# Kernel tuning notes

Hardware: AMD Instinct MI355X
Metric: run time of the kernel (lower is better)

## Reference

```python
import jax, jax.numpy as jnp
import numpy as np

B, S, HID, NH, DH, L, FF = 1, 4096, 768, 12, 64, 12, 3072
WIN = 256       # one-sided sliding window (attention_window = 512 total)
NG = 16         # number of global-attention tokens
VOCAB = 50265
NEG = -1e9


def layer_norm(x, g, b, eps=1e-5):
    mu = jnp.mean(x, -1, keepdims=True)
    var = jnp.mean((x - mu) ** 2, -1, keepdims=True)
    return (x - mu) * jax.lax.rsqrt(var + eps) * g + b


def forward(input_ids, attention_mask, global_attention_mask, tok_emb, pos_emb,
            emb_ln_w, emb_ln_b, Wqkv, bqkv, Wo, bo, ln1_w, ln1_b,
            W1, b1, W2, b2, ln2_w, ln2_b, cls_W, cls_b):
    c = WIN
    nc = S // c
    amask = attention_mask.astype(jnp.float32)          # [B,S]
    gmask = global_attention_mask.astype(jnp.float32)   # [B,S]

    # --- static-shape helpers for the sparse pattern ---
    # key chunk k covers padded positions [k*c, k*c + 3c)
    idx = (jnp.arange(nc) * c)[:, None] + jnp.arange(3 * c)[None, :]      # [nc,3c]
    diff = jnp.arange(3 * c)[None, :] - c - jnp.arange(c)[:, None]        # [c,3c]
    band = jnp.abs(diff) <= c
    mp = jnp.pad(amask, ((0, 0), (c, c)))[:, idx]                         # [B,nc,3c]
    gp = jnp.pad(gmask, ((0, 0), (c, c)))[:, idx]
    key_ok = (mp > 0) & (gp == 0)           # local keys: valid and not global (globals handled separately)
    loc_valid = band[None, None] & key_ok[:, :, None, :]                  # [B,nc,c,3c]

    # indices of the NG global tokens (earliest first)
    _, gidx = jax.lax.top_k(gmask * (2.0 * S) - jnp.arange(S, dtype=jnp.float32), NG)
    gvalid = jnp.take_along_axis(gmask, gidx, axis=1)                     # [B,NG]

    def attn(x, Wqkv_l, bqkv_l, Wo_l, bo_l):
        qkv = x @ Wqkv_l + bqkv_l
        q, k, v = jnp.split(qkv, 3, axis=-1)
        hd = lambda t: t.reshape(B, S, NH, DH).transpose(0, 2, 1, 3)      # [B,nh,S,dh]
        q = hd(q) * (DH ** -0.5); k = hd(k); v = hd(v)

        # sliding-window (banded) attention via overlapping key chunks
        kp = jnp.pad(k, ((0, 0), (0, 0), (c, c), (0, 0)))
        vp = jnp.pad(v, ((0, 0), (0, 0), (c, c), (0, 0)))
        Kc, Vc = kp[:, :, idx], vp[:, :, idx]                             # [B,nh,nc,3c,dh]
        Qc = q.reshape(B, NH, nc, c, DH)
        s_loc = jnp.einsum('bhkpd,bhkqd->bhkpq', Qc, Kc)                  # [B,nh,nc,c,3c]
        s_loc = jnp.where(loc_valid[:, None], s_loc, NEG)

        # every token also attends to the global tokens
        gi = jnp.broadcast_to(gidx[:, None, :, None], (B, NH, NG, DH))
        Kg = jnp.take_along_axis(k, gi, axis=2)                           # [B,nh,NG,dh]
        Vg = jnp.take_along_axis(v, gi, axis=2)
        Qg = jnp.take_along_axis(q, gi, axis=2)
        s_glb = jnp.einsum('bhkpd,bhgd->bhkpg', Qc, Kg)                   # [B,nh,nc,c,NG]
        s_glb = jnp.where(gvalid[:, None, None, None, :] > 0, s_glb, NEG)

        p = jax.nn.softmax(jnp.concatenate([s_loc, s_glb], -1), axis=-1)
        o = (jnp.einsum('bhkpq,bhkqd->bhkpd', p[..., :3 * c], Vc)
             + jnp.einsum('bhkpg,bhgd->bhkpd', p[..., 3 * c:], Vg))
        o = o.reshape(B, NH, S, DH).transpose(0, 2, 1, 3)                 # [B,S,nh,dh]

        # global tokens attend to the full sequence
        s_full = jnp.einsum('bhgd,bhsd->bhgs', Qg, k)
        s_full = jnp.where(amask[:, None, None, :] > 0, s_full, NEG)
        og = jnp.einsum('bhgs,bhsd->bhgd', jax.nn.softmax(s_full, -1), v)
        og = og.transpose(0, 2, 1, 3)                                     # [B,NG,nh,dh]
        bi = jnp.arange(B)[:, None]
        o = o.at[bi, gidx].set(jnp.where(gvalid[..., None, None] > 0, og, o[bi, gidx]))
        return o.reshape(B, S, HID) @ Wo_l + bo_l

    h = layer_norm(tok_emb[input_ids] + pos_emb[None], emb_ln_w, emb_ln_b)

    def step(h, p):
        Wq, bq, Wo_l, bo_l, g1, bl1, w1, bb1, w2, bb2, g2, bl2 = p
        h = layer_norm(h + attn(h, Wq, bq, Wo_l, bo_l), g1, bl1)          # post-LN, RoBERTa-style
        f = jax.nn.gelu(h @ w1 + bb1, approximate=False) @ w2 + bb2
        h = layer_norm(h + f, g2, bl2)
        return h, None

    h, _ = jax.lax.scan(step, h, (Wqkv, bqkv, Wo, bo, ln1_w, ln1_b,
                                  W1, b1, W2, b2, ln2_w, ln2_b))
    m = amask[..., None]
    pooled = (h * m).sum(1) / m.sum(1)           # masked mean-pool; dropout is eval no-op
    return pooled @ cls_W + cls_b                # [B,2] logits


def setup_inputs():
    key = jax.random.key(0)
    ks = jax.random.split(key, 8)
    nrm = lambda k, shp: jax.random.normal(k, shp, jnp.float32) * 0.02
    return dict(
        input_ids=jax.random.randint(ks[0], (B, S), 0, VOCAB),
        attention_mask=jnp.ones((B, S), jnp.int32),
        global_attention_mask=jnp.concatenate(
            [jnp.ones((B, NG), jnp.int32), jnp.zeros((B, S - NG), jnp.int32)], axis=1),
        tok_emb=nrm(ks[1], (VOCAB, HID)),
        pos_emb=nrm(ks[2], (S, HID)),
        emb_ln_w=jnp.ones((HID,)), emb_ln_b=jnp.zeros((HID,)),
        Wqkv=nrm(ks[3], (L, HID, 3 * HID)), bqkv=jnp.zeros((L, 3 * HID)),
        Wo=nrm(ks[4], (L, HID, HID)), bo=jnp.zeros((L, HID)),
        ln1_w=jnp.ones((L, HID)), ln1_b=jnp.zeros((L, HID)),
        W1=nrm(ks[5], (L, HID, FF)), b1=jnp.zeros((L, FF)),
        W2=nrm(ks[6], (L, FF, HID)), b2=jnp.zeros((L, HID)),
        ln2_w=jnp.ones((L, HID)), ln2_b=jnp.zeros((L, HID)),
        cls_W=nrm(ks[7], (HID, 2)), cls_b=jnp.zeros((2,)),
    )


def reference(input_ids, attention_mask, global_attention_mask, tok_emb, pos_emb,
              emb_ln_w, emb_ln_b, Wqkv, bqkv, Wo, bo, ln1_w, ln1_b,
              W1, b1, W2, b2, ln2_w, ln2_b, cls_W, cls_b):
    return forward(input_ids, attention_mask, global_attention_mask, tok_emb, pos_emb,
                   emb_ln_w, emb_ln_b, Wqkv, bqkv, Wo, bo, ln1_w, ln1_b,
                   W1, b1, W2, b2, ln2_w, ln2_b, cls_W, cls_b)
```

## Files before the change

kernel.cpp:

```cpp
#include <hip/hip_runtime.h>
#include <cmath>

#define S 4096
#define HID 768
#define NH 12
#define DH 64
#define CHUNK 256
#define NC (S / CHUNK)
#define NG 16
#define FF 3072
#define NLAYER 12
#define QKV3 (3 * HID)
#define NEGV -1e9f

typedef _Float16 f16;
typedef __attribute__((ext_vector_type(2))) _Float16 f16x2;
typedef __attribute__((ext_vector_type(4))) _Float16 f16x4;
typedef __attribute__((ext_vector_type(8))) _Float16 f16x8;
typedef __attribute__((ext_vector_type(4))) float f32x4;

__device__ __forceinline__ void async16(f16* lds, const f16* g) {
  __builtin_amdgcn_global_load_lds((const __attribute__((address_space(1))) unsigned int*)g,
                                   (__attribute__((address_space(3))) unsigned int*)lds,
                                   16, 0, 0);
}

__device__ __forceinline__ int xcd_swz(int lin, int nwg) {
  return (lin & 7) * (nwg >> 3) + (lin >> 3);
}

__device__ __forceinline__ float block_reduce_sum(float v, float* red) {
  int t = threadIdx.x;
  red[t] = v; __syncthreads();
  for (int st = 128; st > 0; st >>= 1) {
    if (t < st) red[t] += red[t + st];
    __syncthreads();
  }
  float r = red[0]; __syncthreads();
  return r;
}

__global__ void gidx_kernel(const int* __restrict__ gmask, int* __restrict__ gidx,
                            float* __restrict__ gvalid) {
  if (threadIdx.x != 0 || blockIdx.x != 0) return;
  int cnt = 0;
  for (int s = 0; s < S && cnt < NG; s++)
    if (gmask[s] > 0) { gidx[cnt] = s; gvalid[cnt] = 1.f; cnt++; }
  for (int s = 0; s < S && cnt < NG; s++)
    if (gmask[s] == 0) { gidx[cnt] = s; gvalid[cnt] = 0.f; cnt++; }
}

__global__ __launch_bounds__(256) void embed_ln_kernel(
    const int* __restrict__ ids, const float* __restrict__ tok,
    const float* __restrict__ pos, const float* __restrict__ g,
    const float* __restrict__ b, float* __restrict__ h, f16* __restrict__ h16) {
  int s = blockIdx.x, t = threadIdx.x;
  __shared__ float xs[HID];
  __shared__ float red[256];
  const float* tr = tok + (size_t)ids[s] * HID;
  const float* pr = pos + (size_t)s * HID;
  float ls = 0.f;
  for (int i = t; i < HID; i += 256) { float v = tr[i] + pr[i]; xs[i] = v; ls += v; }
  float mu = block_reduce_sum(ls, red) * (1.f / HID);
  float lv = 0.f;
  for (int i = t; i < HID; i += 256) { float d = xs[i] - mu; lv += d * d; }
  float var = block_reduce_sum(lv, red) * (1.f / HID);
  float inv = rsqrtf(var + 1e-5f);
  for (int i = t; i < HID; i += 256) {
    float o = (xs[i] - mu) * inv * g[i] + b[i];
    h[(size_t)s * HID + i] = o;
    h16[(size_t)s * HID + i] = (f16)o;
  }
}

__global__ __launch_bounds__(256) void add_ln_kernel(
    float* __restrict__ h, const f16* __restrict__ x2,
    const float* __restrict__ g, const float* __restrict__ b, f16* __restrict__ h16) {
  int s = blockIdx.x, t = threadIdx.x;
  __shared__ float xs[HID];
  __shared__ float red[256];
  float ls = 0.f;
  for (int i = t; i < HID; i += 256) {
    float v = h[(size_t)s * HID + i] + (float)x2[(size_t)s * HID + i];
    xs[i] = v; ls += v;
  }
  float mu = block_reduce_sum(ls, red) * (1.f / HID);
  float lv = 0.f;
  for (int i = t; i < HID; i += 256) { float d = xs[i] - mu; lv += d * d; }
  float var = block_reduce_sum(lv, red) * (1.f / HID);
  float inv = rsqrtf(var + 1e-5f);
  for (int i = t; i < HID; i += 256) {
    float o = (xs[i] - mu) * inv * g[i] + b[i];
    h[(size_t)s * HID + i] = o;
    h16[(size_t)s * HID + i] = (f16)o;
  }
}

__global__ __launch_bounds__(256) void wt_kernel(const float* __restrict__ W,
                                                 f16* __restrict__ WT, int K, int N) {
  size_t lo = (size_t)blockIdx.z * K * N;
  const float* Wl = W + lo;
  f16* WTl = WT + lo;
  __shared__ float tile[32][33];
  int k0 = blockIdx.y * 32, n0 = blockIdx.x * 32;
  int t = threadIdx.x;
  int r = t >> 3, c = (t & 7) * 4;
  float4 v = *(const float4*)&Wl[(size_t)(k0 + r) * N + n0 + c];
  tile[r][c] = v.x; tile[r][c + 1] = v.y; tile[r][c + 2] = v.z; tile[r][c + 3] = v.w;
  __syncthreads();
  int n = t >> 3, kq = (t & 7) * 4;
  f16x4 o = {(f16)tile[kq][n], (f16)tile[kq + 1][n], (f16)tile[kq + 2][n], (f16)tile[kq + 3][n]};
  *(f16x4*)&WTl[(size_t)(n0 + n) * K + k0 + kq] = o;
}

#define GBK 64

template <int OMODE, bool GELU>
__global__ __launch_bounds__(256) void gemm_f16_kernel(
    const f16* __restrict__ A, const f16* __restrict__ BT,
    const float* __restrict__ bias, void* __restrict__ Cout, int M, int N, int K) {
  __shared__ f16 As[128 * GBK];
  __shared__ f16 Bs[128 * GBK];
  int t = threadIdx.x, lane = t & 63, wave = t >> 6;
  int wr = wave >> 1, wc = wave & 1;
  int gx = gridDim.x;
  int nl = xcd_swz(blockIdx.y * gx + blockIdx.x, gx * gridDim.y);
  int bx = nl % gx, by = nl / gx;

  f32x4 acc[4][4];
#pragma unroll
  for (int mi = 0; mi < 4; mi++)
#pragma unroll
    for (int ni = 0; ni < 4; ni++) acc[mi][ni] = (f32x4){0.f, 0.f, 0.f, 0.f};

  const f16* Ablk = A + (size_t)(by * 128) * K;
  const f16* Bblk = BT + (size_t)(bx * 128) * K;
  int rl = lane >> 3;
  int lc = (lane & 7) ^ rl;

  for (int k0 = 0; k0 < K; k0 += GBK) {
#pragma unroll
    for (int ii = 0; ii < 4; ii++) {
      int i = wave * 4 + ii;
      int r = i * 8 + rl;
      async16(&As[i * 512], Ablk + (size_t)r * K + k0 + lc * 8);
      async16(&Bs[i * 512], Bblk + (size_t)r * K + k0 + lc * 8);
    }
    __syncthreads();
#pragma unroll
    for (int kc = 0; kc < 2; kc++) {
      f16x8 af[4], bf[4];
#pragma unroll
      for (int mi = 0; mi < 4; mi++) {
        int row = wr * 64 + mi * 16 + (lane & 15);
        int pc = (kc * 4 + (lane >> 4)) ^ (row & 7);
        af[mi] = *(const f16x8*)&As[row * 64 + pc * 8];
      }
#pragma unroll
      for (int ni = 0; ni < 4; ni++) {
        int row = wc * 64 + ni * 16 + (lane & 15);
        int pc = (kc * 4 + (lane >> 4)) ^ (row & 7);
        bf[ni] = *(const f16x8*)&Bs[row * 64 + pc * 8];
      }
#pragma unroll
      for (int mi = 0; mi < 4; mi++)
#pragma unroll
        for (int ni = 0; ni < 4; ni++)
          acc[mi][ni] = __builtin_amdgcn_mfma_f32_16x16x32_f16(af[mi], bf[ni], acc[mi][ni], 0, 0, 0);
    }
    __syncthreads();
  }

  int row_base = by * 128 + wr * 64 + (lane >> 4) * 4;
  int col_base = bx * 128 + wc * 64 + (lane & 15);
#pragma unroll
  for (int mi = 0; mi < 4; mi++) {
#pragma unroll
    for (int ni = 0; ni < 4; ni++) {
      int col = col_base + ni * 16;
      float bs = bias[col];
#pragma unroll
      for (int j = 0; j < 4; j++) {
        int row = row_base + mi * 16 + j;
        float x = acc[mi][ni][j] + bs;
        if (GELU) x = 0.5f * x * (1.f + erff(x * 0.70710678118654752f));
        if (OMODE == 0) ((float*)Cout)[(size_t)row * N + col] = x;
        else ((f16*)Cout)[(size_t)row * N + col] = (f16)x;
      }
    }
  }
}

template <int OMODE, bool GELU>
__global__ __launch_bounds__(256) void gemm_f16_n64_kernel(
    const f16* __restrict__ A, const f16* __restrict__ BT,
    const float* __restrict__ bias, void* __restrict__ Cout, int M, int N, int K) {
  __shared__ f16 As[128 * GBK];
  __shared__ f16 Bs[64 * GBK];
  int t = threadIdx.x, lane = t & 63, wave = t >> 6;
  int wr = wave >> 1, wc = wave & 1;
  int gx = gridDim.x;
  int nl = xcd_swz(blockIdx.y * gx + blockIdx.x, gx * gridDim.y);
  int bx = nl % gx, by = nl / gx;

  f32x4 acc[4][2];
#pragma unroll
  for (int mi = 0; mi < 4; mi++)
#pragma unroll
    for (int ni = 0; ni < 2; ni++) acc[mi][ni] = (f32x4){0.f, 0.f, 0.f, 0.f};

  const f16* Ablk = A + (size_t)(by * 128) * K;
  const f16* Bblk = BT + (size_t)(bx * 64) * K;
  int rl = lane >> 3;
  int lc = (lane & 7) ^ rl;

  for (int k0 = 0; k0 < K; k0 += GBK) {
#pragma unroll
    for (int ii = 0; ii < 4; ii++) {
      int i = wave * 4 + ii;
      int r = i * 8 + rl;
      async16(&As[i * 512], Ablk + (size_t)r * K + k0 + lc * 8);
    }
#pragma unroll
    for (int ii = 0; ii < 2; ii++) {
      int i = wave * 2 + ii;
      int r = i * 8 + rl;
      async16(&Bs[i * 512], Bblk + (size_t)r * K + k0 + lc * 8);
    }
    __syncthreads();
#pragma unroll
    for (int kc = 0; kc < 2; kc++) {
      f16x8 af[4], bf[2];
#pragma unroll
      for (int mi = 0; mi < 4; mi++) {
        int row = wr * 64 + mi * 16 + (lane & 15);
        int pc = (kc * 4 + (lane >> 4)) ^ (row & 7);
        af[mi] = *(const f16x8*)&As[row * 64 + pc * 8];
      }
#pragma unroll
      for (int ni = 0; ni < 2; ni++) {
        int row = wc * 32 + ni * 16 + (lane & 15);
        int pc = (kc * 4 + (lane >> 4)) ^ (row & 7);
        bf[ni] = *(const f16x8*)&Bs[row * 64 + pc * 8];
      }
#pragma unroll
      for (int mi = 0; mi < 4; mi++)
#pragma unroll
        for (int ni = 0; ni < 2; ni++)
          acc[mi][ni] = __builtin_amdgcn_mfma_f32_16x16x32_f16(af[mi], bf[ni], acc[mi][ni], 0, 0, 0);
    }
    __syncthreads();
  }

  int row_base = by * 128 + wr * 64 + (lane >> 4) * 4;
  int col_base = bx * 64 + wc * 32 + (lane & 15);
#pragma unroll
  for (int mi = 0; mi < 4; mi++) {
#pragma unroll
    for (int ni = 0; ni < 2; ni++) {
      int col = col_base + ni * 16;
      float bs = bias[col];
#pragma unroll
      for (int j = 0; j < 4; j++) {
        int row = row_base + mi * 16 + j;
        float x = acc[mi][ni][j] + bs;
        if (GELU) x = 0.5f * x * (1.f + erff(x * 0.70710678118654752f));
        if (OMODE == 0) ((float*)Cout)[(size_t)row * N + col] = x;
        else ((f16*)Cout)[(size_t)row * N + col] = (f16)x;
      }
    }
  }
}

#define ROWP 72

__global__ __launch_bounds__(256) void local_attn_mfma_kernel(
    const f16* __restrict__ qkv, const int* __restrict__ amask,
    const int* __restrict__ gmask, const int* __restrict__ gidx,
    const float* __restrict__ gvalid, f16* __restrict__ outp) {
  int nl = xcd_swz(blockIdx.x, NH * 64);
  int h = nl >> 6;
  int qb = nl & 63;
  int q0 = qb * 64;
  int t = threadIdx.x, lane = t & 63, w = t >> 6;
  int g4 = lane >> 4, l15 = lane & 15;

  __shared__ f16 Qs[64 * ROWP];
  __shared__ f16 Kt[64 * ROWP];
  __shared__ f16 Vt[64 * ROWP];
  __shared__ f16 Pb[4 * 16 * ROWP];
  __shared__ unsigned kokLo, kokHi;
  __shared__ float gvs[NG];

  {
    int r = t >> 2, c2 = (t & 3) * 2;
    const f16* qr = qkv + (size_t)(q0 + r) * QKV3 + h * DH + c2 * 8;
    f16x8 v0 = *(const f16x8*)qr;
    f16x8 v1 = *(const f16x8*)(qr + 8);
#pragma unroll
    for (int e = 0; e < 8; e++) { v0[e] = v0[e] * (f16)0.125f; v1[e] = v1[e] * (f16)0.125f; }
    *(f16x8*)&Qs[r * ROWP + c2 * 8] = v0;
    *(f16x8*)&Qs[r * ROWP + c2 * 8 + 8] = v1;
    if (t < NG) gvs[t] = gvalid[t];
  }
  __syncthreads();

  int qrow = w * 16 + l15;
  f16x8 qf0 = *(const f16x8*)&Qs[qrow * ROWP + g4 * 8];
  f16x8 qf1 = *(const f16x8*)&Qs[qrow * ROWP + 32 + g4 * 8];

  float mb = -50000.f, lp = 0.f;
  f32x4 oacc[4];
#pragma unroll
  for (int sd = 0; sd < 4; sd++) oacc[sd] = (f32x4){0.f, 0.f, 0.f, 0.f};

  f16* Pw = &Pb[w * 16 * ROWP];

  for (int kt = 0; kt <= 9; kt++) {
    int jb = q0 - 256 + kt * 64;
    bool isG = (kt == 9);
    if (!isG && (jb + 64 <= 0 || jb >= S)) continue;
    __syncthreads();
    {
      int k = t >> 2, c2 = (t & 3) * 2;
      int j = isG ? (k < NG ? gidx[k] : -1) : (jb + k);
      bool jv = isG ? (k < NG && gvs[k] > 0.f) : (j >= 0 && j < S);
      f16x8 v0 = {}, v1 = {};
      if (jv) {
        const f16* kr = qkv + (size_t)j * QKV3 + HID + h * DH + c2 * 8;
        v0 = *(const f16x8*)kr; v1 = *(const f16x8*)(kr + 8);
      }
      *(f16x8*)&Kt[k * ROWP + c2 * 8] = v0;
      *(f16x8*)&Kt[k * ROWP + c2 * 8 + 8] = v1;
    }
    if (w == 0) {
      int k = lane;
      bool ok;
      if (isG) ok = (k < NG && gvs[k] > 0.f);
      else {
        int j = jb + k;
        ok = (j >= 0 && j < S) && (amask[j] != 0) && (gmask[j] == 0);
      }
      unsigned long long m = __ballot(ok);
      if (lane == 0) { kokLo = (unsigned)m; kokHi = (unsigned)(m >> 32); }
    }
    {
      int k2 = (t & 31) * 2, dq = (t >> 5) * 8;
      int j0 = isG ? (k2 < NG ? gidx[k2] : -1) : (jb + k2);
      int j1 = isG ? (k2 + 1 < NG ? gidx[k2 + 1] : -1) : (jb + k2 + 1);
      bool ok0 = isG ? (k2 < NG && gvs[k2] > 0.f) : (j0 >= 0 && j0 < S);
      bool ok1 = isG ? (k2 + 1 < NG && gvs[k2 + 1] > 0.f) : (j1 >= 0 && j1 < S);
      f16x8 va = {}, vb = {};
      if (ok0) va = *(const f16x8*)(qkv + (size_t)j0 * QKV3 + 2 * HID + h * DH + dq);
      if (ok1) vb = *(const f16x8*)(qkv + (size_t)j1 * QKV3 + 2 * HID + h * DH + dq);
#pragma unroll
      for (int e = 0; e < 8; e++) {
        f16x2 pr = {va[e], vb[e]};
        *(f16x2*)&Vt[(dq + e) * ROWP + k2] = pr;
      }
    }
    __syncthreads();

    unsigned long long kok = ((unsigned long long)kokHi << 32) | (unsigned long long)kokLo;

    f32x4 sv[4];
    __builtin_amdgcn_s_setprio(1);
#pragma unroll
    for (int s4 = 0; s4 < 4; s4++) {
      int krow = s4 * 16 + l15;
      f16x8 ka0 = *(const f16x8*)&Kt[krow * ROWP + g4 * 8];
      f16x8 ka1 = *(const f16x8*)&Kt[krow * ROWP + 32 + g4 * 8];
      f32x4 a = {0.f, 0.f, 0.f, 0.f};
      a = __builtin_amdgcn_mfma_f32_16x16x32_f16(ka0, qf0, a, 0, 0, 0);
      a = __builtin_amdgcn_mfma_f32_16x16x32_f16(ka1, qf1, a, 0, 0, 0);
      sv[s4] = a;
    }
    __builtin_amdgcn_s_setprio(0);
    int ql = w * 16 + l15;
#pragma unroll
    for (int s4 = 0; s4 < 4; s4++)
#pragma unroll
      for (int r = 0; r < 4; r++) {
        int kl = s4 * 16 + g4 * 4 + r;
        bool ok = (kok >> kl) & 1ull;
        if (kt == 0) ok = ok && (kl >= ql);
        else if (kt == 8) ok = ok && (kl <= ql);
        sv[s4][r] = ok ? sv[s4][r] : -1e30f;
      }
    float mt = -1e30f;
#pragma unroll
    for (int s4 = 0; s4 < 4; s4++)
#pragma unroll
      for (int r = 0; r < 4; r++) mt = fmaxf(mt, sv[s4][r]);
    mt = fmaxf(mt, __shfl_xor(mt, 16));
    mt = fmaxf(mt, __shfl_xor(mt, 32));
    float mn = fmaxf(mb, mt);
    float corr = __expf(mb - mn);
    mb = mn;
    lp *= corr;
#pragma unroll
    for (int sd = 0; sd < 4; sd++)
#pragma unroll
      for (int r = 0; r < 4; r++) oacc[sd][r] *= corr;
#pragma unroll
    for (int s4 = 0; s4 < 4; s4++) {
#pragma unroll
      for (int rp = 0; rp < 2; rp++) {
        float p0 = __expf(sv[s4][rp * 2] - mn);
        float p1 = __expf(sv[s4][rp * 2 + 1] - mn);
        f16 h0 = (f16)p0, h1 = (f16)p1;
        lp += (float)h0 + (float)h1;
        int kl = s4 * 16 + g4 * 4 + rp * 2;
        f16x2 pr = {h0, h1};
        *(f16x2*)&Pw[l15 * ROWP + kl] = pr;
      }
    }
    f16x8 pf0 = *(const f16x8*)&Pw[l15 * ROWP + g4 * 8];
    f16x8 pf1 = *(const f16x8*)&Pw[l15 * ROWP + 32 + g4 * 8];
    __builtin_amdgcn_s_setprio(1);
#pragma unroll
    for (int sd = 0; sd < 4; sd++) {
      int drow = sd * 16 + l15;
      f16x8 va0 = *(const f16x8*)&Vt[drow * ROWP + g4 * 8];
      f16x8 va1 = *(const f16x8*)&Vt[drow * ROWP + 32 + g4 * 8];
      oacc[sd] = __builtin_amdgcn_mfma_f32_16x16x32_f16(va0, pf0, oacc[sd], 0, 0, 0);
      oacc[sd] = __builtin_amdgcn_mfma_f32_16x16x32_f16(va1, pf1, oacc[sd], 0, 0, 0);
    }
    __builtin_amdgcn_s_setprio(0);
  }

  float lt = lp + __shfl_xor(lp, 16);
  lt = lt + __shfl_xor(lt, 32);
  float inv = (lt > 0.f) ? 1.f / lt : 0.f;
  int qg = q0 + w * 16 + l15;
  f16* orow = outp + (size_t)qg * HID + h * DH;
#pragma unroll
  for (int sd = 0; sd < 4; sd++)
#pragma unroll
    for (int r = 0; r < 4; r++)
      orow[sd * 16 + g4 * 4 + r] = (f16)(oacc[sd][r] * inv);
}

__global__ __launch_bounds__(256) void gscore_kernel(
    const f16* __restrict__ qkv, const int* __restrict__ amask,
    const int* __restrict__ gidx, float* __restrict__ Sg, float2* __restrict__ cstat) {
  int h = blockIdx.x >> 4, jc = blockIdx.x & 15;
  int t = threadIdx.x, lane = t & 63, w = t >> 6;
  __shared__ f16 Qs[NG][DH];
  __shared__ float wred[4][NG];
  __shared__ float cmaxs[NG];
  if (t < 128) {
    int g = t >> 3, c = (t & 7) * 8;
    const f16* qr = qkv + (size_t)gidx[g] * QKV3 + h * DH + c;
    *(f16x8*)&Qs[g][c] = *(const f16x8*)qr;
  }
  __syncthreads();
  int j = jc * 256 + t;
  const f16x8* kr = (const f16x8*)(qkv + (size_t)j * QKV3 + HID + h * DH);
  f16x8 kv[8];
#pragma unroll
  for (int c = 0; c < 8; c++) kv[c] = kr[c];
  bool ok = amask[j] != 0;
  float sg[NG];
#pragma unroll 4
  for (int g = 0; g < NG; g++) {
    float s = 0.f;
#pragma unroll
    for (int c = 0; c < 8; c++) {
      f16x8 qv = *(const f16x8*)&Qs[g][c * 8];
#pragma unroll
      for (int e = 0; e < 8; e++) s += (float)qv[e] * (float)kv[c][e];
    }
    sg[g] = ok ? s * 0.125f : NEGV;
    Sg[(size_t)(h * NG + g) * S + j] = sg[g];
  }
#pragma unroll
  for (int g = 0; g < NG; g++) {
    float m = sg[g];
#pragma unroll
    for (int st = 1; st < 64; st <<= 1) m = fmaxf(m, __shfl_xor(m, st));
    if (lane == 0) wred[w][g] = m;
  }
  __syncthreads();
  if (t < NG)
    cmaxs[t] = fmaxf(fmaxf(wred[0][t], wred[1][t]), fmaxf(wred[2][t], wred[3][t]));
  __syncthreads();
#pragma unroll
  for (int g = 0; g < NG; g++) {
    float p = __expf(sg[g] - cmaxs[g]);
#pragma unroll
    for (int st = 1; st < 64; st <<= 1) p += __shfl_xor(p, st);
    if (lane == 0) wred[w][g] = p;
  }
  __syncthreads();
  if (t < NG) {
    float s4 = wred[0][t] + wred[1][t] + wred[2][t] + wred[3][t];
    cstat[((size_t)(h * NG + t)) * 16 + jc] = make_float2(cmaxs[t], s4);
  }
}

__global__ __launch_bounds__(256) void gpv_kernel(
    const f16* __restrict__ qkv, const float* __restrict__ Sg,
    const float2* __restrict__ cstat, float* __restrict__ part) {
  int h = blockIdx.x >> 4, jc = blockIdx.x & 15;
  int jb = jc * 256;
  int t = threadIdx.x;
  __shared__ float Ps[NG][256];
  __shared__ f16 Vs[256][DH];
  __shared__ float ms[NG], dinv[NG];
  if (t < NG) {
    const float2* cs = &cstat[((size_t)(h * NG + t)) * 16];
    float m = -1e30f;
#pragma unroll
    for (int c = 0; c < 16; c++) m = fmaxf(m, cs[c].x);
    float den = 0.f;
#pragma unroll
    for (int c = 0; c < 16; c++) den += cs[c].y * __expf(cs[c].x - m);
    ms[t] = m;
    dinv[t] = den > 0.f ? 1.f / den : 0.f;
  }
  __syncthreads();
#pragma unroll
  for (int g = 0; g < NG; g++)
    Ps[g][t] = __expf(Sg[(size_t)(h * NG + g) * S + jb + t] - ms[g]) * dinv[g];
  {
    int r = t >> 3, c = (t & 7) * 8;
#pragma unroll
    for (int pp = 0; pp < 8; pp++) {
      int row = pp * 32 + r;
      const f16* vr = qkv + (size_t)(jb + row) * QKV3 + 2 * HID + h * DH + c;
      *(f16x8*)&Vs[row][c] = *(const f16x8*)vr;
    }
  }
  __syncthreads();
  int d = t & 63, g4 = t >> 6;
  float o0 = 0.f, o1 = 0.f, o2 = 0.f, o3 = 0.f;
#pragma unroll 8
  for (int j = 0; j < 256; j++) {
    float v = (float)Vs[j][d];
    o0 += Ps[g4][j] * v;
    o1 += Ps[g4 + 4][j] * v;
    o2 += Ps[g4 + 8][j] * v;
    o3 += Ps[g4 + 12][j] * v;
  }
  size_t base = ((size_t)h * NG) * 16 * 64;
  part[base + ((size_t)(g4) * 16 + jc) * 64 + d] = o0;
  part[base + ((size_t)(g4 + 4) * 16 + jc) * 64 + d] = o1;
  part[base + ((size_t)(g4 + 8) * 16 + jc) * 64 + d] = o2;
  part[base + ((size_t)(g4 + 12) * 16 + jc) * 64 + d] = o3;
}

__global__ __launch_bounds__(64) void gout_kernel(
    const float* __restrict__ part, const int* __restrict__ gidx,
    const float* __restrict__ gvalid, f16* __restrict__ attn16) {
  int h = blockIdx.x >> 4, g = blockIdx.x & 15;
  if (gvalid[g] <= 0.f) return;
  int d = threadIdx.x;
  const float* pr = part + (((size_t)(h * NG + g)) * 16) * 64 + d;
  float s = 0.f;
#pragma unroll
  for (int jc = 0; jc < 16; jc++) s += pr[jc * 64];
  attn16[(size_t)gidx[g] * HID + h * DH + d] = (f16)s;
}

__global__ __launch_bounds__(256) void pool_part_kernel(
    const float* __restrict__ h, const int* __restrict__ amask, float* __restrict__ part) {
  int b = blockIdx.x, t = threadIdx.x;
  float a0 = 0.f, a1 = 0.f, a2 = 0.f;
  for (int r = 0; r < 64; r++) {
    int s = b * 64 + r;
    float w = (float)amask[s];
    const float* hr = h + (size_t)s * HID;
    a0 += hr[t] * w;
    a1 += hr[t + 256] * w;
    a2 += hr[t + 512] * w;
  }
  part[(size_t)b * HID + t] = a0;
  part[(size_t)b * HID + t + 256] = a1;
  part[(size_t)b * HID + t + 512] = a2;
}

__global__ __launch_bounds__(256) void cls_head_kernel(
    const float* __restrict__ part, const int* __restrict__ amask,
    const float* __restrict__ clsW, const float* __restrict__ clsb,
    float* __restrict__ out) {
  __shared__ float pooled[HID];
  __shared__ float red[256];
  int t = threadIdx.x;
  for (int i = t; i < HID; i += 256) {
    float s = 0.f;
    for (int b2 = 0; b2 < 64; b2++) s += part[(size_t)b2 * HID + i];
    pooled[i] = s;
  }
  float c = 0.f;
  for (int s2 = t; s2 < S; s2 += 256) c += (float)amask[s2];
  float cnt = block_reduce_sum(c, red);
  float p0 = 0.f, p1 = 0.f;
  for (int i = t; i < HID; i += 256) {
    float pv = pooled[i] / cnt;
    p0 += pv * clsW[i * 2];
    p1 += pv * clsW[i * 2 + 1];
  }
  float s0 = block_reduce_sum(p0, red);
  float s1 = block_reduce_sum(p1, red);
  if (t == 0) { out[0] = s0 + clsb[0]; out[1] = s1 + clsb[1]; }
}

extern "C" void kernel_launch(void* const* d_in, const int* in_sizes, int n_in,
                              void* d_out, int out_size, void* d_ws, size_t ws_size,
                              hipStream_t stream) {
  const int* ids = (const int*)d_in[0];
  const int* amask = (const int*)d_in[1];
  const int* gmask = (const int*)d_in[2];
  const float* tok = (const float*)d_in[3];
  const float* pos = (const float*)d_in[4];
  const float* elnw = (const float*)d_in[5];
  const float* elnb = (const float*)d_in[6];
  const float* Wqkv = (const float*)d_in[7];
  const float* bqkv = (const float*)d_in[8];
  const float* Wo = (const float*)d_in[9];
  const float* bo = (const float*)d_in[10];
  const float* ln1w = (const float*)d_in[11];
  const float* ln1b = (const float*)d_in[12];
  const float* W1 = (const float*)d_in[13];
  const float* b1 = (const float*)d_in[14];
  const float* W2 = (const float*)d_in[15];
  const float* b2 = (const float*)d_in[16];
  const float* ln2w = (const float*)d_in[17];
  const float* ln2b = (const float*)d_in[18];
  const float* clsW = (const float*)d_in[19];
  const float* clsb = (const float*)d_in[20];

  char* w8 = (char*)d_ws;
  size_t o = 0;
  float* h = (float*)(w8 + o); o += (size_t)S * HID * 4;
  f16* h16 = (f16*)(w8 + o); o += (size_t)S * HID * 2;
  f16* qkv16 = (f16*)(w8 + o); o += (size_t)S * QKV3 * 2;
  f16* attn16 = (f16*)(w8 + o); o += (size_t)S * HID * 2;
  f16* ff16 = (f16*)(w8 + o); o += (size_t)S * FF * 2;
  f16* proj16 = (f16*)(w8 + o); o += (size_t)S * HID * 2;
  float* part = (float*)(w8 + o); o += (size_t)64 * HID * 4;
  int* gidx = (int*)(w8 + o); o += 64;
  float* gvalid = (float*)(w8 + o); o += 64;
  f16* WqkvT = (f16*)(w8 + o); o += (size_t)NLAYER * HID * QKV3 * 2;
  f16* WoT = (f16*)(w8 + o); o += (size_t)NLAYER * HID * HID * 2;
  f16* W1T = (f16*)(w8 + o); o += (size_t)NLAYER * HID * FF * 2;
  f16* W2T = (f16*)(w8 + o); o += (size_t)NLAYER * FF * HID * 2;
  float* Sg = (float*)(w8 + o); o += (size_t)NH * NG * S * 4;
  float2* cstat = (float2*)(w8 + o); o += (size_t)NH * NG * 16 * 8;
  float* gpart = (float*)(w8 + o); o += (size_t)NH * NG * 16 * 64 * 4;

  gidx_kernel<<<1, 64, 0, stream>>>(gmask, gidx, gvalid);
  embed_ln_kernel<<<S, 256, 0, stream>>>(ids, tok, pos, elnw, elnb, h, h16);
  wt_kernel<<<dim3(QKV3 / 32, HID / 32, NLAYER), 256, 0, stream>>>(Wqkv, WqkvT, HID, QKV3);
  wt_kernel<<<dim3(HID / 32, HID / 32, NLAYER), 256, 0, stream>>>(Wo, WoT, HID, HID);
  wt_kernel<<<dim3(FF / 32, HID / 32, NLAYER), 256, 0, stream>>>(W1, W1T, HID, FF);
  wt_kernel<<<dim3(HID / 32, FF / 32, NLAYER), 256, 0, stream>>>(W2, W2T, FF, HID);

  for (int l = 0; l < NLAYER; l++) {
    gemm_f16_kernel<1, false><<<dim3(QKV3 / 128, S / 128), 256, 0, stream>>>(
        h16, WqkvT + (size_t)l * HID * QKV3, bqkv + (size_t)l * QKV3, qkv16, S, QKV3, HID);
    local_attn_mfma_kernel<<<NH * 64, 256, 0, stream>>>(
        qkv16, amask, gmask, gidx, gvalid, attn16);
    gscore_kernel<<<NH * 16, 256, 0, stream>>>(qkv16, amask, gidx, Sg, cstat);
    gpv_kernel<<<NH * 16, 256, 0, stream>>>(qkv16, Sg, cstat, gpart);
    gout_kernel<<<NH * NG, 64, 0, stream>>>(gpart, gidx, gvalid, attn16);
    gemm_f16_n64_kernel<1, false><<<dim3(HID / 64, S / 128), 256, 0, stream>>>(
        attn16, WoT + (size_t)l * HID * HID, bo + (size_t)l * HID, proj16, S, HID, HID);
    add_ln_kernel<<<S, 256, 0, stream>>>(h, proj16, ln1w + (size_t)l * HID,
                                         ln1b + (size_t)l * HID, h16);
    gemm_f16_kernel<1, true><<<dim3(FF / 128, S / 128), 256, 0, stream>>>(
        h16, W1T + (size_t)l * HID * FF, b1 + (size_t)l * FF, ff16, S, FF, HID);
    gemm_f16_n64_kernel<1, false><<<dim3(HID / 64, S / 128), 256, 0, stream>>>(
        ff16, W2T + (size_t)l * FF * HID, b2 + (size_t)l * HID, proj16, S, HID, FF);
    add_ln_kernel<<<S, 256, 0, stream>>>(h, proj16, ln2w + (size_t)l * HID,
                                         ln2b + (size_t)l * HID, h16);
  }
  pool_part_kernel<<<64, 256, 0, stream>>>(h, amask, part);
  cls_head_kernel<<<1, 256, 0, stream>>>(part, amask, clsW, clsb, (float*)d_out);
}
```

Baseline: 2.586 ms.

## Fuse residual into GEMM epilogue, merge attention kernels, drop fp32 hidden state

The residual add moves into the output-projection and FFN-down GEMM epilogues, and the fp32 hidden-state buffer is removed, so LayerNorm reads one fp16 sum. Local attention and global score computation now share one launch with a block-index split. The global PV and output reduction merge into one kernel that loops over all chunks per (head, global token). This removes several launches and the fp32 traffic, but holding the residual stream in fp16 across 12 layers adds rounding error, and the merged global PV kernel has less parallelism.

```diff
diff --git a/kernel.cpp b/kernel.cpp
--- a/kernel.cpp
+++ b/kernel.cpp
@@ -53,7 +53,7 @@
 __global__ __launch_bounds__(256) void embed_ln_kernel(
     const int* __restrict__ ids, const float* __restrict__ tok,
     const float* __restrict__ pos, const float* __restrict__ g,
-    const float* __restrict__ b, float* __restrict__ h, f16* __restrict__ h16) {
+    const float* __restrict__ b, f16* __restrict__ h16) {
   int s = blockIdx.x, t = threadIdx.x;
   __shared__ float xs[HID];
   __shared__ float red[256];
@@ -66,34 +66,25 @@
   for (int i = t; i < HID; i += 256) { float d = xs[i] - mu; lv += d * d; }
   float var = block_reduce_sum(lv, red) * (1.f / HID);
   float inv = rsqrtf(var + 1e-5f);
-  for (int i = t; i < HID; i += 256) {
-    float o = (xs[i] - mu) * inv * g[i] + b[i];
-    h[(size_t)s * HID + i] = o;
-    h16[(size_t)s * HID + i] = (f16)o;
-  }
-}
-
-__global__ __launch_bounds__(256) void add_ln_kernel(
-    float* __restrict__ h, const f16* __restrict__ x2,
-    const float* __restrict__ g, const float* __restrict__ b, f16* __restrict__ h16) {
+  for (int i = t; i < HID; i += 256)
+    h16[(size_t)s * HID + i] = (f16)((xs[i] - mu) * inv * g[i] + b[i]);
+}
+
+__global__ __launch_bounds__(256) void ln_kernel(
+    const f16* __restrict__ sum16, const float* __restrict__ g,
+    const float* __restrict__ b, f16* __restrict__ h16) {
   int s = blockIdx.x, t = threadIdx.x;
-  __shared__ float xs[HID];
   __shared__ float red[256];
-  float ls = 0.f;
-  for (int i = t; i < HID; i += 256) {
-    float v = h[(size_t)s * HID + i] + (float)x2[(size_t)s * HID + i];
-    xs[i] = v; ls += v;
-  }
-  float mu = block_reduce_sum(ls, red) * (1.f / HID);
-  float lv = 0.f;
-  for (int i = t; i < HID; i += 256) { float d = xs[i] - mu; lv += d * d; }
-  float var = block_reduce_sum(lv, red) * (1.f / HID);
+  float x0 = (float)sum16[(size_t)s * HID + t];
+  float x1 = (float)sum16[(size_t)s * HID + t + 256];
+  float x2 = (float)sum16[(size_t)s * HID + t + 512];
+  float mu = block_reduce_sum(x0 + x1 + x2, red) * (1.f / HID);
+  float d0 = x0 - mu, d1 = x1 - mu, d2 = x2 - mu;
+  float var = block_reduce_sum(d0 * d0 + d1 * d1 + d2 * d2, red) * (1.f / HID);
   float inv = rsqrtf(var + 1e-5f);
-  for (int i = t; i < HID; i += 256) {
-    float o = (xs[i] - mu) * inv * g[i] + b[i];
-    h[(size_t)s * HID + i] = o;
-    h16[(size_t)s * HID + i] = (f16)o;
-  }
+  h16[(size_t)s * HID + t] = (f16)(d0 * inv * g[t] + b[t]);
+  h16[(size_t)s * HID + t + 256] = (f16)(d1 * inv * g[t + 256] + b[t + 256]);
+  h16[(size_t)s * HID + t + 512] = (f16)(d2 * inv * g[t + 512] + b[t + 512]);
 }
 
 __global__ __launch_bounds__(256) void wt_kernel(const float* __restrict__ W,
@@ -115,10 +106,10 @@
 
 #define GBK 64
 
-template <int OMODE, bool GELU>
+template <bool GELU>
 __global__ __launch_bounds__(256) void gemm_f16_kernel(
     const f16* __restrict__ A, const f16* __restrict__ BT,
-    const float* __restrict__ bias, void* __restrict__ Cout, int M, int N, int K) {
+    const float* __restrict__ bias, f16* __restrict__ Cout, int M, int N, int K) {
   __shared__ f16 As[128 * GBK];
   __shared__ f16 Bs[128 * GBK];
   int t = threadIdx.x, lane = t & 63, wave = t >> 6;
@@ -184,17 +175,17 @@
         int row = row_base + mi * 16 + j;
         float x = acc[mi][ni][j] + bs;
         if (GELU) x = 0.5f * x * (1.f + erff(x * 0.70710678118654752f));
-        if (OMODE == 0) ((float*)Cout)[(size_t)row * N + col] = x;
-        else ((f16*)Cout)[(size_t)row * N + col] = (f16)x;
-      }
-    }
-  }
-}
-
-template <int OMODE, bool GELU>
+        Cout[(size_t)row * N + col] = (f16)x;
+      }
+    }
+  }
+}
+
+template <bool RESID>
 __global__ __launch_bounds__(256) void gemm_f16_n64_kernel(
     const f16* __restrict__ A, const f16* __restrict__ BT,
-    const float* __restrict__ bias, void* __restrict__ Cout, int M, int N, int K) {
+    const float* __restrict__ bias, const f16* __restrict__ resid,
+    f16* __restrict__ Cout, int M, int N, int K) {
   __shared__ f16 As[128 * GBK];
   __shared__ f16 Bs[64 * GBK];
   int t = threadIdx.x, lane = t & 63, wave = t >> 6;
@@ -264,316 +255,305 @@
       for (int j = 0; j < 4; j++) {
         int row = row_base + mi * 16 + j;
         float x = acc[mi][ni][j] + bs;
-        if (GELU) x = 0.5f * x * (1.f + erff(x * 0.70710678118654752f));
-        if (OMODE == 0) ((float*)Cout)[(size_t)row * N + col] = x;
-        else ((f16*)Cout)[(size_t)row * N + col] = (f16)x;
+        if (RESID) x += (float)resid[(size_t)row * N + col];
+        Cout[(size_t)row * N + col] = (f16)x;
       }
     }
   }
 }
 
 #define ROWP 72
-
-__global__ __launch_bounds__(256) void local_attn_mfma_kernel(
+#define SMEM_HALVES (4 * 4608 + 64)
+
+__global__ __launch_bounds__(256) void attn_fused_kernel(
     const f16* __restrict__ qkv, const int* __restrict__ amask,
     const int* __restrict__ gmask, const int* __restrict__ gidx,
-    const float* __restrict__ gvalid, f16* __restrict__ outp) {
-  int nl = xcd_swz(blockIdx.x, NH * 64);
-  int h = nl >> 6;
-  int qb = nl & 63;
-  int q0 = qb * 64;
+    const float* __restrict__ gvalid, f16* __restrict__ outp,
+    float* __restrict__ Sg, float2* __restrict__ cstat) {
+  __shared__ __align__(16) f16 smem[SMEM_HALVES];
+  int bid = blockIdx.x;
   int t = threadIdx.x, lane = t & 63, w = t >> 6;
-  int g4 = lane >> 4, l15 = lane & 15;
-
-  __shared__ f16 Qs[64 * ROWP];
-  __shared__ f16 Kt[64 * ROWP];
-  __shared__ f16 Vt[64 * ROWP];
-  __shared__ f16 Pb[4 * 16 * ROWP];
-  __shared__ unsigned kokLo, kokHi;
-  __shared__ float gvs[NG];
-
-  {
-    int r = t >> 2, c2 = (t & 3) * 2;
-    const f16* qr = qkv + (size_t)(q0 + r) * QKV3 + h * DH + c2 * 8;
-    f16x8 v0 = *(const f16x8*)qr;
-    f16x8 v1 = *(const f16x8*)(qr + 8);
-#pragma unroll
-    for (int e = 0; e < 8; e++) { v0[e] = v0[e] * (f16)0.125f; v1[e] = v1[e] * (f16)0.125f; }
-    *(f16x8*)&Qs[r * ROWP + c2 * 8] = v0;
-    *(f16x8*)&Qs[r * ROWP + c2 * 8 + 8] = v1;
-    if (t < NG) gvs[t] = gvalid[t];
-  }
-  __syncthreads();
-
-  int qrow = w * 16 + l15;
-  f16x8 qf0 = *(const f16x8*)&Qs[qrow * ROWP + g4 * 8];
-  f16x8 qf1 = *(const f16x8*)&Qs[qrow * ROWP + 32 + g4 * 8];
-
-  float mb = -50000.f, lp = 0.f;
-  f32x4 oacc[4];
-#pragma unroll
-  for (int sd = 0; sd < 4; sd++) oacc[sd] = (f32x4){0.f, 0.f, 0.f, 0.f};
-
-  f16* Pw = &Pb[w * 16 * ROWP];
-
-  for (int kt = 0; kt <= 9; kt++) {
-    int jb = q0 - 256 + kt * 64;
-    bool isG = (kt == 9);
-    if (!isG && (jb + 64 <= 0 || jb >= S)) continue;
-    __syncthreads();
+
+  if (bid < NH * 64) {
+    int nl = xcd_swz(bid, NH * 64);
+    int h = nl >> 6, qb = nl & 63;
+    int q0 = qb * 64;
+    int g4 = lane >> 4, l15 = lane & 15;
+
+    f16* Qs = smem;
+    f16* Kt = smem + 4608;
+    f16* Vt = smem + 2 * 4608;
+    f16* Pb = smem + 3 * 4608;
+    float* gvs = (float*)(smem + 4 * 4608);
+    unsigned* kokp = (unsigned*)(gvs + NG);
+
     {
-      int k = t >> 2, c2 = (t & 3) * 2;
-      int j = isG ? (k < NG ? gidx[k] : -1) : (jb + k);
-      bool jv = isG ? (k < NG && gvs[k] > 0.f) : (j >= 0 && j < S);
-      f16x8 v0 = {}, v1 = {};
-      if (jv) {
-        const f16* kr = qkv + (size_t)j * QKV3 + HID + h * DH + c2 * 8;
-        v0 = *(const f16x8*)kr; v1 = *(const f16x8*)(kr + 8);
-      }
-      *(f16x8*)&Kt[k * ROWP + c2 * 8] = v0;
-      *(f16x8*)&Kt[k * ROWP + c2 * 8 + 8] = v1;
-    }
-    if (w == 0) {
-      int k = lane;
-      bool ok;
-      if (isG) ok = (k < NG && gvs[k] > 0.f);
-      else {
-        int j = jb + k;
-        ok = (j >= 0 && j < S) && (amask[j] != 0) && (gmask[j] == 0);
-      }
-      unsigned long long m = __ballot(ok);
-      if (lane == 0) { kokLo = (unsigned)m; kokHi = (unsigned)(m >> 32); }
-    }
-    {
-      int k2 = (t & 31) * 2, dq = (t >> 5) * 8;
-      int j0 = isG ? (k2 < NG ? gidx[k2] : -1) : (jb + k2);
-      int j1 = isG ? (k2 + 1 < NG ? gidx[k2 + 1] : -1) : (jb + k2 + 1);
-      bool ok0 = isG ? (k2 < NG && gvs[k2] > 0.f) : (j0 >= 0 && j0 < S);
-      bool ok1 = isG ? (k2 + 1 < NG && gvs[k2 + 1] > 0.f) : (j1 >= 0 && j1 < S);
-      f16x8 va = {}, vb = {};
-      if (ok0) va = *(const f16x8*)(qkv + (size_t)j0 * QKV3 + 2 * HID + h * DH + dq);
-      if (ok1) vb = *(const f16x8*)(qkv + (size_t)j1 * QKV3 + 2 * HID + h * DH + dq);
-#pragma unroll
-      for (int e = 0; e < 8; e++) {
-        f16x2 pr = {va[e], vb[e]};
-        *(f16x2*)&Vt[(dq + e) * ROWP + k2] = pr;
-      }
-    }
-    __syncthreads();
-
-    unsigned long long kok = ((unsigned long long)kokHi << 32) | (unsigned long long)kokLo;
-
-    f32x4 sv[4];
-    __builtin_amdgcn_s_setprio(1);
-#pragma unroll
-    for (int s4 = 0; s4 < 4; s4++) {
-      int krow = s4 * 16 + l15;
-      f16x8 ka0 = *(const f16x8*)&Kt[krow * ROWP + g4 * 8];
-      f16x8 ka1 = *(const f16x8*)&Kt[krow * ROWP + 32 + g4 * 8];
-      f32x4 a = {0.f, 0.f, 0.f, 0.f};
-      a = __builtin_amdgcn_mfma_f32_16x16x32_f16(ka0, qf0, a, 0, 0, 0);
-      a = __builtin_amdgcn_mfma_f32_16x16x32_f16(ka1, qf1, a, 0, 0, 0);
-      sv[s4] = a;
-    }
-    __builtin_amdgcn_s_setprio(0);
-    int ql = w * 16 + l15;
-#pragma unroll
-    for (int s4 = 0; s4 < 4; s4++)
-#pragma unroll
-      for (int r = 0; r < 4; r++) {
-        int kl = s4 * 16 + g4 * 4 + r;
-        bool ok = (kok >> kl) & 1ull;
-        if (kt == 0) ok = ok && (kl >= ql);
-        else if (kt == 8) ok = ok && (kl <= ql);
-        sv[s4][r] = ok ? sv[s4][r] : -1e30f;
-      }
-    float mt = -1e30f;
-#pragma unroll
-    for (int s4 = 0; s4 < 4; s4++)
-#pragma unroll
-      for (int r = 0; r < 4; r++) mt = fmaxf(mt, sv[s4][r]);
-    mt = fmaxf(mt, __shfl_xor(mt, 16));
-    mt = fmaxf(mt, __shfl_xor(mt, 32));
-    float mn = fmaxf(mb, mt);
-    float corr = __expf(mb - mn);
-    mb = mn;
-    lp *= corr;
+      int r = t >> 2, c2 = (t & 3) * 2;
+      const f16* qr = qkv + (size_t)(q0 + r) * QKV3 + h * DH + c2 * 8;
+      f16x8 v0 = *(const f16x8*)qr;
+      f16x8 v1 = *(const f16x8*)(qr + 8);
+#pragma unroll
+      for (int e = 0; e < 8; e++) { v0[e] = v0[e] * (f16)0.125f; v1[e] = v1[e] * (f16)0.125f; }
+      *(f16x8*)&Qs[r * ROWP + c2 * 8] = v0;
+      *(f16x8*)&Qs[r * ROWP + c2 * 8 + 8] = v1;
+      if (t < NG) gvs[t] = gvalid[t];
+    }
+    __syncthreads();
+
+    int qrow = w * 16 + l15;
+    f16x8 qf0 = *(const f16x8*)&Qs[qrow * ROWP + g4 * 8];
+    f16x8 qf1 = *(const f16x8*)&Qs[qrow * ROWP + 32 + g4 * 8];
+
+    float mb = -50000.f, lp = 0.f;
+    f32x4 oacc[4];
+#pragma unroll
+    for (int sd = 0; sd < 4; sd++) oacc[sd] = (f32x4){0.f, 0.f, 0.f, 0.f};
+
+    f16* Pw = &Pb[w * 16 * ROWP];
+
+    for (int kt = 0; kt <= 9; kt++) {
+      int jb = q0 - 256 + kt * 64;
+      bool isG = (kt == 9);
+      if (!isG && (jb + 64 <= 0 || jb >= S)) continue;
+      __syncthreads();
+      {
+        int k = t >> 2, c2 = (t & 3) * 2;
+        int j = isG ? (k < NG ? gidx[k] : -1) : (jb + k);
+        bool jv = isG ? (k < NG && gvs[k] > 0.f) : (j >= 0 && j < S);
+        f16x8 v0 = {}, v1 = {};
+        if (jv) {
+          const f16* kr = qkv + (size_t)j * QKV3 + HID + h * DH + c2 * 8;
+          v0 = *(const f16x8*)kr; v1 = *(const f16x8*)(kr + 8);
+        }
+        *(f16x8*)&Kt[k * ROWP + c2 * 8] = v0;
+        *(f16x8*)&Kt[k * ROWP + c2 * 8 + 8] = v1;
+      }
+      if (w == 0) {
+        int k = lane;
+        bool ok;
+        if (isG) ok = (k < NG && gvs[k] > 0.f);
+        else {
+          int j = jb + k;
+          ok = (j >= 0 && j < S) && (amask[j] != 0) && (gmask[j] == 0);
+        }
+        unsigned long long m = __ballot(ok);
+        if (lane == 0) { kokp[0] = (unsigned)m; kokp[1] = (unsigned)(m >> 32); }
+      }
+      {
+        int k2 = (t & 31) * 2, dq = (t >> 5) * 8;
+        int j0 = isG ? (k2 < NG ? gidx[k2] : -1) : (jb + k2);
+        int j1 = isG ? (k2 + 1 < NG ? gidx[k2 + 1] : -1) : (jb + k2 + 1);
+        bool ok0 = isG ? (k2 < NG && gvs[k2] > 0.f) : (j0 >= 0 && j0 < S);
+        bool ok1 = isG ? (k2 + 1 < NG && gvs[k2 + 1] > 0.f) : (j1 >= 0 && j1 < S);
+        f16x8 va = {}, vb = {};
+        if (ok0) va = *(const f16x8*)(qkv + (size_t)j0 * QKV3 + 2 * HID + h * DH + dq);
+        if (ok1) vb = *(const f16x8*)(qkv + (size_t)j1 * QKV3 + 2 * HID + h * DH + dq);
+#pragma unroll
+        for (int e = 0; e < 8; e++) {
+          f16x2 pr = {va[e], vb[e]};
+          *(f16x2*)&Vt[(dq + e) * ROWP + k2] = pr;
+        }
+      }
+      __syncthreads();
+
+      unsigned long long kok = ((unsigned long long)kokp[1] << 32) | (unsigned long long)kokp[0];
+
+      f32x4 sv[4];
+      __builtin_amdgcn_s_setprio(1);
+#pragma unroll
+      for (int s4 = 0; s4 < 4; s4++) {
+        int krow = s4 * 16 + l15;
+        f16x8 ka0 = *(const f16x8*)&Kt[krow * ROWP + g4 * 8];
+        f16x8 ka1 = *(const f16x8*)&Kt[krow * ROWP + 32 + g4 * 8];
+        f32x4 a = {0.f, 0.f, 0.f, 0.f};
+        a = __builtin_amdgcn_mfma_f32_16x16x32_f16(ka0, qf0, a, 0, 0, 0);
+        a = __builtin_amdgcn_mfma_f32_16x16x32_f16(ka1, qf1, a, 0, 0, 0);
+        sv[s4] = a;
+      }
+      __builtin_amdgcn_s_setprio(0);
+      int ql = w * 16 + l15;
+#pragma unroll
+      for (int s4 = 0; s4 < 4; s4++)
+#pragma unroll
+        for (int r = 0; r < 4; r++) {
+          int kl = s4 * 16 + g4 * 4 + r;
+          bool ok = (kok >> kl) & 1ull;
+          if (kt == 0) ok = ok && (kl >= ql);
+          else if (kt == 8) ok = ok && (kl <= ql);
+          sv[s4][r] = ok ? sv[s4][r] : -1e30f;
+        }
+      float mt = -1e30f;
+#pragma unroll
+      for (int s4 = 0; s4 < 4; s4++)
+#pragma unroll
+        for (int r = 0; r < 4; r++) mt = fmaxf(mt, sv[s4][r]);
+      mt = fmaxf(mt, __shfl_xor(mt, 16));
+      mt = fmaxf(mt, __shfl_xor(mt, 32));
+      float mn = fmaxf(mb, mt);
+      float corr = __expf(mb - mn);
+      mb = mn;
+      lp *= corr;
+#pragma unroll
+      for (int sd = 0; sd < 4; sd++)
+#pragma unroll
+        for (int r = 0; r < 4; r++) oacc[sd][r] *= corr;
+#pragma unroll
+      for (int s4 = 0; s4 < 4; s4++) {
+#pragma unroll
+        for (int rp = 0; rp < 2; rp++) {
+          float p0 = __expf(sv[s4][rp * 2] - mn);
+          float p1 = __expf(sv[s4][rp * 2 + 1] - mn);
+          f16 h0 = (f16)p0, h1 = (f16)p1;
+          lp += (float)h0 + (float)h1;
+          int kl = s4 * 16 + g4 * 4 + rp * 2;
+          f16x2 pr = {h0, h1};
+          *(f16x2*)&Pw[l15 * ROWP + kl] = pr;
+        }
+      }
+      f16x8 pf0 = *(const f16x8*)&Pw[l15 * ROWP + g4 * 8];
+      f16x8 pf1 = *(const f16x8*)&Pw[l15 * ROWP + 32 + g4 * 8];
+      __builtin_amdgcn_s_setprio(1);
+#pragma unroll
+      for (int sd = 0; sd < 4; sd++) {
+        int drow = sd * 16 + l15;
+        f16x8 va0 = *(const f16x8*)&Vt[drow * ROWP + g4 * 8];
+        f16x8 va1 = *(const f16x8*)&Vt[drow * ROWP + 32 + g4 * 8];
+        oacc[sd] = __builtin_amdgcn_mfma_f32_16x16x32_f16(va0, pf0, oacc[sd], 0, 0, 0);
+        oacc[sd] = __builtin_amdgcn_mfma_f32_16x16x32_f16(va1, pf1, oacc[sd], 0, 0, 0);
+      }
+      __builtin_amdgcn_s_setprio(0);
+    }
+
+    float lt = lp + __shfl_xor(lp, 16);
+    lt = lt + __shfl_xor(lt, 32);
+    float inv = (lt > 0.f) ? 1.f / lt : 0.f;
+    int qg = q0 + w * 16 + l15;
+    f16* orow = outp + (size_t)qg * HID + h * DH;
 #pragma unroll
     for (int sd = 0; sd < 4; sd++)
 #pragma unroll
-      for (int r = 0; r < 4; r++) oacc[sd][r] *= corr;
-#pragma unroll
-    for (int s4 = 0; s4 < 4; s4++) {
-#pragma unroll
-      for (int rp = 0; rp < 2; rp++) {
-        float p0 = __expf(sv[s4][rp * 2] - mn);
-        float p1 = __expf(sv[s4][rp * 2 + 1] - mn);
-        f16 h0 = (f16)p0, h1 = (f16)p1;
-        lp += (float)h0 + (float)h1;
-        int kl = s4 * 16 + g4 * 4 + rp * 2;
-        f16x2 pr = {h0, h1};
-        *(f16x2*)&Pw[l15 * ROWP + kl] = pr;
-      }
-    }
-    f16x8 pf0 = *(const f16x8*)&Pw[l15 * ROWP + g4 * 8];
-    f16x8 pf1 = *(const f16x8*)&Pw[l15 * ROWP + 32 + g4 * 8];
-    __builtin_amdgcn_s_setprio(1);
-#pragma unroll
-    for (int sd = 0; sd < 4; sd++) {
-      int drow = sd * 16 + l15;
-      f16x8 va0 = *(const f16x8*)&Vt[drow * ROWP + g4 * 8];
-      f16x8 va1 = *(const f16x8*)&Vt[drow * ROWP + 32 + g4 * 8];
-      oacc[sd] = __builtin_amdgcn_mfma_f32_16x16x32_f16(va0, pf0, oacc[sd], 0, 0, 0);
-      oacc[sd] = __builtin_amdgcn_mfma_f32_16x16x32_f16(va1, pf1, oacc[sd], 0, 0, 0);
-    }
-    __builtin_amdgcn_s_setprio(0);
-  }
-
-  float lt = lp + __shfl_xor(lp, 16);
-  lt = lt + __shfl_xor(lt, 32);
-  float inv = (lt > 0.f) ? 1.f / lt : 0.f;
-  int qg = q0 + w * 16 + l15;
-  f16* orow = outp + (size_t)qg * HID + h * DH;
-#pragma unroll
-  for (int sd = 0; sd < 4; sd++)
-#pragma unroll
-    for (int r = 0; r < 4; r++)
-      orow[sd * 16 + g4 * 4 + r] = (f16)(oacc[sd][r] * inv);
-}
-
-__global__ __launch_bounds__(256) void gscore_kernel(
-    const f16* __restrict__ qkv, const int* __restrict__ amask,
-    const int* __restrict__ gidx, float* __restrict__ Sg, float2* __restrict__ cstat) {
-  int h = blockIdx.x >> 4, jc = blockIdx.x & 15;
-  int t = threadIdx.x, lane = t & 63, w = t >> 6;
-  __shared__ f16 Qs[NG][DH];
-  __shared__ float wred[4][NG];
-  __shared__ float cmaxs[NG];
-  if (t < 128) {
-    int g = t >> 3, c = (t & 7) * 8;
-    const f16* qr = qkv + (size_t)gidx[g] * QKV3 + h * DH + c;
-    *(f16x8*)&Qs[g][c] = *(const f16x8*)qr;
-  }
-  __syncthreads();
-  int j = jc * 256 + t;
-  const f16x8* kr = (const f16x8*)(qkv + (size_t)j * QKV3 + HID + h * DH);
-  f16x8 kv[8];
-#pragma unroll
-  for (int c = 0; c < 8; c++) kv[c] = kr[c];
-  bool ok = amask[j] != 0;
-  float sg[NG];
+      for (int r = 0; r < 4; r++)
+        orow[sd * 16 + g4 * 4 + r] = (f16)(oacc[sd][r] * inv);
+  } else {
+    int gb = bid - NH * 64;
+    int h = gb >> 4, jc = gb & 15;
+    f16* Qs = smem;
+    float* wred = (float*)(smem + NG * DH);
+    float* cmaxs = wred + 4 * NG;
+    if (t < 128) {
+      int g = t >> 3, c = (t & 7) * 8;
+      const f16* qr = qkv + (size_t)gidx[g] * QKV3 + h * DH + c;
+      *(f16x8*)&Qs[g * DH + c] = *(const f16x8*)qr;
+    }
+    __syncthreads();
+    int j = jc * 256 + t;
+    const f16x8* kr = (const f16x8*)(qkv + (size_t)j * QKV3 + HID + h * DH);
+    f16x8 kv[8];
+#pragma unroll
+    for (int c = 0; c < 8; c++) kv[c] = kr[c];
+    bool ok = amask[j] != 0;
+    float sg[NG];
 #pragma unroll 4
-  for (int g = 0; g < NG; g++) {
-    float s = 0.f;
-#pragma unroll
-    for (int c = 0; c < 8; c++) {
-      f16x8 qv = *(const f16x8*)&Qs[g][c * 8];
-#pragma unroll
-      for (int e = 0; e < 8; e++) s += (float)qv[e] * (float)kv[c][e];
-    }
-    sg[g] = ok ? s * 0.125f : NEGV;
-    Sg[(size_t)(h * NG + g) * S + j] = sg[g];
-  }
-#pragma unroll
-  for (int g = 0; g < NG; g++) {
-    float m = sg[g];
-#pragma unroll
-    for (int st = 1; st < 64; st <<= 1) m = fmaxf(m, __shfl_xor(m, st));
-    if (lane == 0) wred[w][g] = m;
-  }
-  __syncthreads();
-  if (t < NG)
-    cmaxs[t] = fmaxf(fmaxf(wred[0][t], wred[1][t]), fmaxf(wred[2][t], wred[3][t]));
-  __syncthreads();
-#pragma unroll
-  for (int g = 0; g < NG; g++) {
-    float p = __expf(sg[g] - cmaxs[g]);
-#pragma unroll
-    for (int st = 1; st < 64; st <<= 1) p += __shfl_xor(p, st);
-    if (lane == 0) wred[w][g] = p;
-  }
-  __syncthreads();
-  if (t < NG) {
-    float s4 = wred[0][t] + wred[1][t] + wred[2][t] + wred[3][t];
-    cstat[((size_t)(h * NG + t)) * 16 + jc] = make_float2(cmaxs[t], s4);
-  }
-}
-
-__global__ __launch_bounds__(256) void gpv_kernel(
+    for (int g = 0; g < NG; g++) {
+      float s = 0.f;
+#pragma unroll
+      for (int c = 0; c < 8; c++) {
+        f16x8 qv = *(const f16x8*)&Qs[g * DH + c * 8];
+#pragma unroll
+        for (int e = 0; e < 8; e++) s += (float)qv[e] * (float)kv[c][e];
+      }
+      sg[g] = ok ? s * 0.125f : NEGV;
+      Sg[(size_t)(h * NG + g) * S + j] = sg[g];
+    }
+#pragma unroll
+    for (int g = 0; g < NG; g++) {
+      float m = sg[g];
+#pragma unroll
+      for (int st = 1; st < 64; st <<= 1) m = fmaxf(m, __shfl_xor(m, st));
+      if (lane == 0) wred[w * NG + g] = m;
+    }
+    __syncthreads();
+    if (t < NG)
+      cmaxs[t] = fmaxf(fmaxf(wred[t], wred[NG + t]), fmaxf(wred[2 * NG + t], wred[3 * NG + t]));
+    __syncthreads();
+#pragma unroll
+    for (int g = 0; g < NG; g++) {
+      float p = __expf(sg[g] - cmaxs[g]);
+#pragma unroll
+      for (int st = 1; st < 64; st <<= 1) p += __shfl_xor(p, st);
+      if (lane == 0) wred[w * NG + g] = p;
+    }
+    __syncthreads();
+    if (t < NG) {
+      float s4 = wred[t] + wred[NG + t] + wred[2 * NG + t] + wred[3 * NG + t];
+      cstat[((size_t)(h * NG + t)) * 16 + jc] = make_float2(cmaxs[t], s4);
+    }
+  }
+}
+
+__global__ __launch_bounds__(256) void gpv2_kernel(
     const f16* __restrict__ qkv, const float* __restrict__ Sg,
-    const float2* __restrict__ cstat, float* __restrict__ part) {
-  int h = blockIdx.x >> 4, jc = blockIdx.x & 15;
-  int jb = jc * 256;
-  int t = threadIdx.x;
-  __shared__ float Ps[NG][256];
-  __shared__ f16 Vs[256][DH];
-  __shared__ float ms[NG], dinv[NG];
-  if (t < NG) {
-    const float2* cs = &cstat[((size_t)(h * NG + t)) * 16];
-    float m = -1e30f;
-#pragma unroll
-    for (int c = 0; c < 16; c++) m = fmaxf(m, cs[c].x);
-    float den = 0.f;
-#pragma unroll
-    for (int c = 0; c < 16; c++) den += cs[c].y * __expf(cs[c].x - m);
-    ms[t] = m;
-    dinv[t] = den > 0.f ? 1.f / den : 0.f;
-  }
-  __syncthreads();
-#pragma unroll
-  for (int g = 0; g < NG; g++)
-    Ps[g][t] = __expf(Sg[(size_t)(h * NG + g) * S + jb + t] - ms[g]) * dinv[g];
-  {
-    int r = t >> 3, c = (t & 7) * 8;
-#pragma unroll
-    for (int pp = 0; pp < 8; pp++) {
-      int row = pp * 32 + r;
-      const f16* vr = qkv + (size_t)(jb + row) * QKV3 + 2 * HID + h * DH + c;
-      *(f16x8*)&Vs[row][c] = *(const f16x8*)vr;
-    }
-  }
-  __syncthreads();
-  int d = t & 63, g4 = t >> 6;
-  float o0 = 0.f, o1 = 0.f, o2 = 0.f, o3 = 0.f;
-#pragma unroll 8
-  for (int j = 0; j < 256; j++) {
-    float v = (float)Vs[j][d];
-    o0 += Ps[g4][j] * v;
-    o1 += Ps[g4 + 4][j] * v;
-    o2 += Ps[g4 + 8][j] * v;
-    o3 += Ps[g4 + 12][j] * v;
-  }
-  size_t base = ((size_t)h * NG) * 16 * 64;
-  part[base + ((size_t)(g4) * 16 + jc) * 64 + d] = o0;
-  part[base + ((size_t)(g4 + 4) * 16 + jc) * 64 + d] = o1;
-  part[base + ((size_t)(g4 + 8) * 16 + jc) * 64 + d] = o2;
-  part[base + ((size_t)(g4 + 12) * 16 + jc) * 64 + d] = o3;
-}
-
-__global__ __launch_bounds__(64) void gout_kernel(
-    const float* __restrict__ part, const int* __restrict__ gidx,
+    const float2* __restrict__ cstat, const int* __restrict__ gidx,
     const float* __restrict__ gvalid, f16* __restrict__ attn16) {
   int h = blockIdx.x >> 4, g = blockIdx.x & 15;
   if (gvalid[g] <= 0.f) return;
-  int d = threadIdx.x;
-  const float* pr = part + (((size_t)(h * NG + g)) * 16) * 64 + d;
-  float s = 0.f;
-#pragma unroll
-  for (int jc = 0; jc < 16; jc++) s += pr[jc * 64];
-  attn16[(size_t)gidx[g] * HID + h * DH + d] = (f16)s;
+  int hg = h * NG + g;
+  int t = threadIdx.x;
+  __shared__ float Ps[256];
+  __shared__ f16 Vs[256][DH];
+  __shared__ float red[256];
+  __shared__ float msh, dinvh;
+  if (t == 0) {
+    const float2* cs = &cstat[(size_t)hg * 16];
+    float m = -1e30f;
+#pragma unroll
+    for (int c = 0; c < 16; c++) m = fmaxf(m, cs[c].x);
+    float den = 0.f;
+#pragma unroll
+    for (int c = 0; c < 16; c++) den += cs[c].y * __expf(cs[c].x - m);
+    msh = m;
+    dinvh = den > 0.f ? 1.f / den : 0.f;
+  }
+  __syncthreads();
+  float m = msh, dinv = dinvh;
+  int d = t & 63, grp = t >> 6;
+  float o = 0.f;
+  for (int jc = 0; jc < 16; jc++) {
+    int jb = jc * 256;
+    Ps[t] = __expf(Sg[(size_t)hg * S + jb + t] - m) * dinv;
+    {
+      int r = t >> 3, c = (t & 7) * 8;
+#pragma unroll
+      for (int pp = 0; pp < 8; pp++) {
+        int row = pp * 32 + r;
+        const f16* vr = qkv + (size_t)(jb + row) * QKV3 + 2 * HID + h * DH + c;
+        *(f16x8*)&Vs[row][c] = *(const f16x8*)vr;
+      }
+    }
+    __syncthreads();
+#pragma unroll 8
+    for (int j = grp; j < 256; j += 4) o += Ps[j] * (float)Vs[j][d];
+    __syncthreads();
+  }
+  red[grp * 64 + d] = o;
+  __syncthreads();
+  if (t < 64) {
+    float oo = red[t] + red[64 + t] + red[128 + t] + red[192 + t];
+    attn16[(size_t)gidx[g] * HID + h * DH + t] = (f16)oo;
+  }
 }
 
 __global__ __launch_bounds__(256) void pool_part_kernel(
-    const float* __restrict__ h, const int* __restrict__ amask, float* __restrict__ part) {
+    const f16* __restrict__ h, const int* __restrict__ amask, float* __restrict__ part) {
   int b = blockIdx.x, t = threadIdx.x;
   float a0 = 0.f, a1 = 0.f, a2 = 0.f;
   for (int r = 0; r < 64; r++) {
     int s = b * 64 + r;
     float w = (float)amask[s];
-    const float* hr = h + (size_t)s * HID;
-    a0 += hr[t] * w;
-    a1 += hr[t + 256] * w;
-    a2 += hr[t + 512] * w;
+    const f16* hr = h + (size_t)s * HID;
+    a0 += (float)hr[t] * w;
+    a1 += (float)hr[t + 256] * w;
+    a2 += (float)hr[t + 512] * w;
   }
   part[(size_t)b * HID + t] = a0;
   part[(size_t)b * HID + t + 256] = a1;
@@ -633,12 +613,11 @@
 
   char* w8 = (char*)d_ws;
   size_t o = 0;
-  float* h = (float*)(w8 + o); o += (size_t)S * HID * 4;
   f16* h16 = (f16*)(w8 + o); o += (size_t)S * HID * 2;
   f16* qkv16 = (f16*)(w8 + o); o += (size_t)S * QKV3 * 2;
   f16* attn16 = (f16*)(w8 + o); o += (size_t)S * HID * 2;
   f16* ff16 = (f16*)(w8 + o); o += (size_t)S * FF * 2;
-  f16* proj16 = (f16*)(w8 + o); o += (size_t)S * HID * 2;
+  f16* sum16 = (f16*)(w8 + o); o += (size_t)S * HID * 2;
   float* part = (float*)(w8 + o); o += (size_t)64 * HID * 4;
   int* gidx = (int*)(w8 + o); o += 64;
   float* gvalid = (float*)(w8 + o); o += 64;
@@ -648,34 +627,29 @@
   f16* W2T = (f16*)(w8 + o); o += (size_t)NLAYER * FF * HID * 2;
   float* Sg = (float*)(w8 + o); o += (size_t)NH * NG * S * 4;
   float2* cstat = (float2*)(w8 + o); o += (size_t)NH * NG * 16 * 8;
-  float* gpart = (float*)(w8 + o); o += (size_t)NH * NG * 16 * 64 * 4;
 
   gidx_kernel<<<1, 64, 0, stream>>>(gmask, gidx, gvalid);
-  embed_ln_kernel<<<S, 256, 0, stream>>>(ids, tok, pos, elnw, elnb, h, h16);
+  embed_ln_kernel<<<S, 256, 0, stream>>>(ids, tok, pos, elnw, elnb, h16);
   wt_kernel<<<dim3(QKV3 / 32, HID / 32, NLAYER), 256, 0, stream>>>(Wqkv, WqkvT, HID, QKV3);
   wt_kernel<<<dim3(HID / 32, HID / 32, NLAYER), 256, 0, stream>>>(Wo, WoT, HID, HID);
   wt_kernel<<<dim3(FF / 32, HID / 32, NLAYER), 256, 0, stream>>>(W1, W1T, HID, FF);
   wt_kernel<<<dim3(HID / 32, FF / 32, NLAYER), 256, 0, stream>>>(W2, W2T, FF, HID);
 
   for (int l = 0; l < NLAYER; l++) {
-    gemm_f16_kernel<1, false><<<dim3(QKV3 / 128, S / 128), 256, 0, stream>>>(
+    gemm_f16_kernel<false><<<dim3(QKV3 / 128, S / 128), 256, 0, stream>>>(
         h16, WqkvT + (size_t)l * HID * QKV3, bqkv + (size_t)l * QKV3, qkv16, S, QKV3, HID);
-    local_attn_mfma_kernel<<<NH * 64, 256, 0, stream>>>(
-        qkv16, amask, gmask, gidx, gvalid, attn16);
-    gscore_kernel<<<NH * 16, 256, 0, stream>>>(qkv16, amask, gidx, Sg, cstat);
-    gpv_kernel<<<NH * 16, 256, 0, stream>>>(qkv16, Sg, cstat, gpart);
-    gout_kernel<<<NH * NG, 64, 0, stream>>>(gpart, gidx, gvalid, attn16);
-    gemm_f16_n64_kernel<1, false><<<dim3(HID / 64, S / 128), 256, 0, stream>>>(
-        attn16, WoT + (size_t)l * HID * HID, bo + (size_t)l * HID, proj16, S, HID, HID);
-    add_ln_kernel<<<S, 256, 0, stream>>>(h, proj16, ln1w + (size_t)l * HID,
-                                         ln1b + (size_t)l * HID, h16);
-    gemm_f16_kernel<1, true><<<dim3(FF / 128, S / 128), 256, 0, stream>>>(
+    attn_fused_kernel<<<NH * 64 + NH * 16, 256, 0, stream>>>(
+        qkv16, amask, gmask, gidx, gvalid, attn16, Sg, cstat);
+    gpv2_kernel<<<NH * NG, 256, 0, stream>>>(qkv16, Sg, cstat, gidx, gvalid, attn16);
+    gemm_f16_n64_kernel<true><<<dim3(HID / 64, S / 128), 256, 0, stream>>>(
+        attn16, WoT + (size_t)l * HID * HID, bo + (size_t)l * HID, h16, sum16, S, HID, HID);
+    ln_kernel<<<S, 256, 0, stream>>>(sum16, ln1w + (size_t)l * HID, ln1b + (size_t)l * HID, h16);
+    gemm_f16_kernel<true><<<dim3(FF / 128, S / 128), 256, 0, stream>>>(
         h16, W1T + (size_t)l * HID * FF, b1 + (size_t)l * FF, ff16, S, FF, HID);
-    gemm_f16_n64_kernel<1, false><<<dim3(HID / 64, S / 128), 256, 0, stream>>>(
-        ff16, W2T + (size_t)l * FF * HID, b2 + (size_t)l * HID, proj16, S, HID, FF);
-    add_ln_kernel<<<S, 256, 0, stream>>>(h, proj16, ln2w + (size_t)l * HID,
-                                         ln2b + (size_t)l * HID, h16);
-  }
-  pool_part_kernel<<<64, 256, 0, stream>>>(h, amask, part);
+    gemm_f16_n64_kernel<true><<<dim3(HID / 64, S / 128), 256, 0, stream>>>(
+        ff16, W2T + (size_t)l * FF * HID, b2 + (size_t)l * HID, h16, sum16, S, HID, FF);
+    ln_kernel<<<S, 256, 0, stream>>>(sum16, ln2w + (size_t)l * HID, ln2b + (size_t)l * HID, h16);
+  }
+  pool_part_kernel<<<64, 256, 0, stream>>>(h16, amask, part);
   cls_head_kernel<<<1, 256, 0, stream>>>(part, amask, clsW, clsb, (float*)d_out);
 }
```

Result: slower. 2.699 ms (+4.4%).
